# Kernel tuning notes

Hardware: AMD Instinct MI355X
Metric: run time of the kernel (lower is better)

The kernel has to match this reference:

```python
import jax, jax.numpy as jnp
import numpy as np

EPS = 1.1920929e-07  # torch fp32 RMSNorm default eps

def rmsnorm(x, w):
    return x * jax.lax.rsqrt(jnp.mean(x * x, axis=-1, keepdims=True) + EPS) * w

def causal_conv1d(x, w, b):
    # x: [B, L, di], w: [di, dc] depthwise kernel, b: [di]
    di, dc = w.shape
    xt = jnp.swapaxes(x, 1, 2)                       # [B, di, L]
    xt = jnp.pad(xt, ((0, 0), (0, 0), (dc - 1, 0)))  # causal left pad
    out = jax.lax.conv_general_dilated(
        xt, w[:, None, :], window_strides=(1,), padding='VALID',
        feature_group_count=di, dimension_numbers=('NCH', 'OIH', 'NCH'))
    return jnp.swapaxes(out + b[None, :, None], 1, 2)  # [B, L, di]

def selective_scan(u, dt, Bm, Cm, A, Dp):
    # u, dt: [B, L, di]; Bm, Cm: [B, L, ds]; A: [di, ds]; Dp: [di]
    Bsz, L, di = u.shape
    ds = A.shape[1]
    def step(h, inp):
        dt_t, B_t, C_t, u_t = inp
        dA = jnp.exp(dt_t[..., None] * A)                           # [B, di, ds]
        dBu = dt_t[..., None] * B_t[:, None, :] * u_t[..., None]    # [B, di, ds]
        h = dA * h + dBu
        y = jnp.einsum('bds,bs->bd', h, C_t)
        return h, y
    h0 = jnp.zeros((Bsz, di, ds), u.dtype)
    xs = (jnp.swapaxes(dt, 0, 1), jnp.swapaxes(Bm, 0, 1),
          jnp.swapaxes(Cm, 0, 1), jnp.swapaxes(u, 0, 1))
    _, ys = jax.lax.scan(step, h0, xs)                # ys: [L, B, di]
    return jnp.swapaxes(ys, 0, 1) + u * Dp            # skip connection D*u

def mamba_block(x, in_w, cw, cb, xp_w, dtp_w, dtp_b, a_log, dp, out_w, d_state, dt_rank):
    di = a_log.shape[0]
    xz = jnp.einsum('bld,ed->ble', x, in_w)           # [B, L, 2*di]
    x_in, z = xz[..., :di], xz[..., di:]
    xc = jax.nn.silu(causal_conv1d(x_in, cw, cb))     # [B, L, di]
    x_dbl = jnp.einsum('bld,ed->ble', xc, xp_w)       # [B, L, dt_rank+2*ds]
    dt = x_dbl[..., :dt_rank]
    Bm = x_dbl[..., dt_rank:dt_rank + d_state]
    Cm = x_dbl[..., dt_rank + d_state:]
    dt = jax.nn.softplus(jnp.einsum('blr,dr->bld', dt, dtp_w) + dtp_b)
    A = -jnp.exp(a_log)                               # [di, ds]
    y = selective_scan(xc, dt, Bm, Cm, A, dp)
    y = y * jax.nn.silu(z)
    return jnp.einsum('bld,ed->ble', y, out_w)        # [B, L, d_model]

def mlp(x, w1, b1, w2, b2):
    h = jax.nn.gelu(jnp.einsum('bld,ed->ble', x, w1) + b1, approximate=False)
    return jax.nn.gelu(jnp.einsum('ble,de->bld', h, w2) + b2, approximate=False)

def reference(x, in_proj_w, conv_w, conv_b, x_proj_w, dt_proj_w, dt_proj_b,
              A_log, D_param, out_proj_w, mlp_w1, mlp_b1, mlp_w2, mlp_b2,
              ln_w, ln2_w):
    d_state = A_log.shape[-1]
    dt_rank = dt_proj_w.shape[-1]
    num_layers = in_proj_w.shape[0]
    residual2 = x
    for i in range(num_layers):
        residual = x
        x = mamba_block(x, in_proj_w[i], conv_w[i], conv_b[i], x_proj_w[i],
                        dt_proj_w[i], dt_proj_b[i], A_log[i], D_param[i],
                        out_proj_w[i], d_state, dt_rank)
        x = mlp(x, mlp_w1, mlp_b1, mlp_w2, mlp_b2)
        x = rmsnorm(x + residual, ln_w)
    return rmsnorm(x + residual2, ln2_w)

def setup_inputs() -> dict:
    key = jax.random.key(0)
    ks = jax.random.split(key, 16)
    B, L, D = 4, 2048, 1024
    NL, di, ds, dc, dtr = 2, 2048, 16, 4, 64
    s = 0.02
    return {
        'x': jax.random.normal(ks[0], (B, L, D), jnp.float32),
        'in_proj_w': jax.random.normal(ks[1], (NL, 2 * di, D), jnp.float32) * s,
        'conv_w': jax.random.normal(ks[2], (NL, di, dc), jnp.float32) * 0.3,
        'conv_b': jax.random.normal(ks[3], (NL, di), jnp.float32) * 0.02,
        'x_proj_w': jax.random.normal(ks[4], (NL, dtr + 2 * ds, di), jnp.float32) * s,
        'dt_proj_w': jax.random.normal(ks[5], (NL, di, dtr), jnp.float32) * 0.1,
        'dt_proj_b': jax.random.normal(ks[6], (NL, di), jnp.float32) * 0.5 - 4.0,
        'A_log': jnp.log(jax.random.uniform(ks[7], (NL, di, ds), jnp.float32, 1.0, 16.0)),
        'D_param': jax.random.normal(ks[8], (NL, di), jnp.float32),
        'out_proj_w': jax.random.normal(ks[9], (NL, D, di), jnp.float32) * s,
        'mlp_w1': jax.random.normal(ks[10], (2 * D, D), jnp.float32) * s,
        'mlp_b1': jnp.zeros((2 * D,), jnp.float32),
        'mlp_w2': jax.random.normal(ks[11], (D, 2 * D), jnp.float32) * s,
        'mlp_b2': jnp.zeros((D,), jnp.float32),
        'ln_w': jnp.ones((D,), jnp.float32),
        'ln2_w': jnp.ones((D,), jnp.float32),
    }
```

## Files before the change

### kernel.cpp

```cpp
#include <hip/hip_runtime.h>
#include <math.h>

namespace {

constexpr int Bsz = 4;
constexpr int L   = 2048;
constexpr int D   = 1024;
constexpr int DI  = 2048;
constexpr int DSTATE = 16;
constexpr int DTR = 64;
constexpr int ML  = Bsz * L;
constexpr int NCH = 32;
constexpr int CL  = 64;

typedef __attribute__((ext_vector_type(8))) short bfrag;
typedef __attribute__((ext_vector_type(4))) float f32x4;

__device__ __forceinline__ unsigned short f2b(float f) {
  union { float f; unsigned int u; } c; c.f = f;
  unsigned int u = c.u;
  unsigned int r = (u + 0x7fffu + ((u >> 16) & 1u)) >> 16;
  return (unsigned short)r;
}
__device__ __forceinline__ float b2f(unsigned short h) {
  union { unsigned int u; float f; } c; c.u = ((unsigned int)h) << 16;
  return c.f;
}

__device__ __forceinline__ void async16(const void* g, void* l) {
  __builtin_amdgcn_global_load_lds(
      (const __attribute__((address_space(1))) void*)g,
      (__attribute__((address_space(3))) void*)l, 16, 0, 0);
}

template<int ACT>
__device__ __forceinline__ float activate(float x) {
  if (ACT == 1) { return x / (1.f + expf(-x)); }
  if (ACT == 2) { return 0.5f * x * (1.f + erff(x * 0.7071067811865475f)); }
  if (ACT == 3) { return (x > 20.f) ? x : log1pf(expf(x)); }
  return x;
}

template<int ACT, bool HAS_BIAS, int BN, bool SPLIT>
__global__ __launch_bounds__(512) void gemm2(
    const unsigned short* __restrict__ A, long lda,
    const unsigned short* __restrict__ W, long ldw,
    const float* __restrict__ bias,
    unsigned short* __restrict__ C0,
    unsigned short* __restrict__ C1,
    long ldc, int K)
{
  constexpr int NB   = BN / 64;
  constexpr int ABUF = 256 * 64;
  constexpr int BBUF = BN * 64;
  constexpr int NLA  = 4;
  constexpr int NLB  = NB;
  constexpr int NL   = NLA + NLB;
  __shared__ unsigned short lds[2 * ABUF + 2 * BBUF];

  const int tid  = threadIdx.x;
  const int lane = tid & 63;
  const int wid  = tid >> 6;
  const int wr   = wid >> 2;
  const int wc   = wid & 3;
  const int frow = lane & 15;
  const int klg  = lane >> 4;

  const int gx = gridDim.x;
  int id = blockIdx.y * gx + blockIdx.x;
  const int q = (gx * gridDim.y) >> 3;
  id = (id & 7) * q + (id >> 3);
  const int bx = id % gx;
  const int by = id / gx;
  const long bm = (long)by * 256;
  const long bn = (long)bx * BN;

  unsigned short* Cb;
  long cbase;
  if (SPLIT) {
    if (bn < 2048) { Cb = C0; cbase = bn; }
    else           { Cb = C1; cbase = bn - 2048; }
  } else { Cb = C0; cbase = bn; }

  f32x4 acc[8][NB];
  #pragma unroll
  for (int m = 0; m < 8; ++m)
    #pragma unroll
    for (int n = 0; n < NB; ++n)
      acc[m][n] = (f32x4){0.f, 0.f, 0.f, 0.f};

  auto stage = [&](int kt, int p) {
    const long kcol = (long)kt * 64;
    #pragma unroll
    for (int l = 0; l < NLA; ++l) {
      const int idx = tid + l * 512;
      const int row = idx >> 3;
      const int ch  = (idx & 7) ^ (row & 7);
      async16(A + (bm + row) * lda + kcol + ch * 8,
              &lds[p * ABUF + idx * 8]);
    }
    #pragma unroll
    for (int l = 0; l < NLB; ++l) {
      const int idx = tid + l * 512;
      const int row = idx >> 3;
      const int ch  = (idx & 7) ^ (row & 7);
      async16(W + (bn + row) * ldw + kcol + ch * 8,
              &lds[2 * ABUF + p * BBUF + idx * 8]);
    }
  };

  const int NT = K >> 6;
  stage(0, 0);
  stage(1, 1);
  asm volatile("s_waitcnt vmcnt(%0)" :: "n"(NL) : "memory");
  __builtin_amdgcn_sched_barrier(0);
  __builtin_amdgcn_s_barrier();

  for (int kt = 0; kt < NT; ++kt) {
    const unsigned short* Ab = &lds[(kt & 1) * ABUF];
    const unsigned short* Bb = &lds[2 * ABUF + (kt & 1) * BBUF];
    __builtin_amdgcn_s_setprio(1);
    #pragma unroll
    for (int kk = 0; kk < 2; ++kk) {
      bfrag av[8], bv[NB];
      #pragma unroll
      for (int m = 0; m < 8; ++m) {
        const int r  = wr * 128 + m * 16 + frow;
        const int ch = (kk * 4 + klg) ^ (r & 7);
        av[m] = *reinterpret_cast<const bfrag*>(&Ab[r * 64 + ch * 8]);
      }
      #pragma unroll
      for (int n = 0; n < NB; ++n) {
        const int r  = wc * (BN / 4) + n * 16 + frow;
        const int ch = (kk * 4 + klg) ^ (r & 7);
        bv[n] = *reinterpret_cast<const bfrag*>(&Bb[r * 64 + ch * 8]);
      }
      #pragma unroll
      for (int m = 0; m < 8; ++m)
        #pragma unroll
        for (int n = 0; n < NB; ++n)
          acc[m][n] = __builtin_amdgcn_mfma_f32_16x16x32_bf16(bv[n], av[m], acc[m][n], 0, 0, 0);
    }
    __builtin_amdgcn_s_setprio(0);
    if (kt + 1 == NT) break;
    __builtin_amdgcn_sched_barrier(0);
    __builtin_amdgcn_s_barrier();
    if (kt + 2 < NT) {
      stage(kt + 2, kt & 1);
      asm volatile("s_waitcnt vmcnt(%0)" :: "n"(NL) : "memory");
    } else {
      asm volatile("s_waitcnt vmcnt(0)" ::: "memory");
    }
    __builtin_amdgcn_sched_barrier(0);
    __builtin_amdgcn_s_barrier();
  }

  #pragma unroll
  for (int n = 0; n < NB; ++n) {
    const long coff = wc * (BN / 4) + n * 16 + klg * 4;
    float4 b4 = make_float4(0.f, 0.f, 0.f, 0.f);
    if (HAS_BIAS) b4 = *reinterpret_cast<const float4*>(&bias[bn + coff]);
    #pragma unroll
    for (int m = 0; m < 8; ++m) {
      const long row = bm + wr * 128 + m * 16 + frow;
      const float v0 = activate<ACT>(acc[m][n][0] + b4.x);
      const float v1 = activate<ACT>(acc[m][n][1] + b4.y);
      const float v2 = activate<ACT>(acc[m][n][2] + b4.z);
      const float v3 = activate<ACT>(acc[m][n][3] + b4.w);
      ushort4 o; o.x = f2b(v0); o.y = f2b(v1); o.z = f2b(v2); o.w = f2b(v3);
      *reinterpret_cast<ushort4*>(&Cb[row * ldc + cbase + coff]) = o;
    }
  }
}

template<int ACT, bool HAS_BIAS>
__global__ __launch_bounds__(256) void gemm_mfma(
    const unsigned short* __restrict__ A, long lda,
    const unsigned short* __restrict__ W, long ldw,
    const float* __restrict__ bias,
    unsigned short* __restrict__ C, long ldc,
    int K)
{
  __shared__ unsigned short As[128 * 32];
  __shared__ unsigned short Bs[128 * 32];
  const int tid  = threadIdx.x;
  const int lane = tid & 63;
  const int w    = tid >> 6;
  const int wr   = w >> 1, wc = w & 1;
  const long bm = (long)blockIdx.y * 128;
  const long bn = (long)blockIdx.x * 128;

  const int srow = tid >> 2;
  const int scol = (tid & 3) * 8;
  const unsigned short* ga0 = A + (bm + srow)      * lda + scol;
  const unsigned short* ga1 = A + (bm + 64 + srow) * lda + scol;
  const unsigned short* gb0 = W + (bn + srow)      * ldw + scol;
  const unsigned short* gb1 = W + (bn + 64 + srow) * ldw + scol;
  char* lA = (char*)As;
  char* lB = (char*)Bs;
  const int loff = tid * 16;

  const int frow = lane & 15;
  const int klg  = lane >> 4;
  const int fko  = klg * 8;

  f32x4 acc[4][4];
  #pragma unroll
  for (int m = 0; m < 4; ++m)
    #pragma unroll
    for (int n = 0; n < 4; ++n)
      acc[m][n] = (f32x4){0.f, 0.f, 0.f, 0.f};

  for (int k0 = 0; k0 < K; k0 += 32) {
    __syncthreads();
    async16(ga0 + k0, lA + loff);
    async16(ga1 + k0, lA + 4096 + loff);
    async16(gb0 + k0, lB + loff);
    async16(gb1 + k0, lB + 4096 + loff);
    __syncthreads();
    bfrag a[4], b[4];
    #pragma unroll
    for (int m = 0; m < 4; ++m)
      a[m] = *reinterpret_cast<const bfrag*>(&As[(wr*64 + m*16 + frow)*32 + fko]);
    #pragma unroll
    for (int n = 0; n < 4; ++n)
      b[n] = *reinterpret_cast<const bfrag*>(&Bs[(wc*64 + n*16 + frow)*32 + fko]);
    #pragma unroll
    for (int m = 0; m < 4; ++m)
      #pragma unroll
      for (int n = 0; n < 4; ++n)
        acc[m][n] = __builtin_amdgcn_mfma_f32_16x16x32_bf16(b[n], a[m], acc[m][n], 0, 0, 0);
  }

  #pragma unroll
  for (int n = 0; n < 4; ++n) {
    const long col = bn + wc*64 + n*16 + klg*4;
    float4 b4 = make_float4(0.f, 0.f, 0.f, 0.f);
    if (HAS_BIAS) b4 = *reinterpret_cast<const float4*>(&bias[col]);
    #pragma unroll
    for (int m = 0; m < 4; ++m) {
      const long row = bm + wr*64 + m*16 + frow;
      const float v0 = activate<ACT>(acc[m][n][0] + b4.x);
      const float v1 = activate<ACT>(acc[m][n][1] + b4.y);
      const float v2 = activate<ACT>(acc[m][n][2] + b4.z);
      const float v3 = activate<ACT>(acc[m][n][3] + b4.w);
      ushort4 o; o.x = f2b(v0); o.y = f2b(v1); o.z = f2b(v2); o.w = f2b(v3);
      *reinterpret_cast<ushort4*>(&C[row * ldc + col]) = o;
    }
  }
}

__global__ __launch_bounds__(256) void xproj_mfma(
    const unsigned short* __restrict__ A,
    const unsigned short* __restrict__ W,
    float* __restrict__ xdbl,
    unsigned short* __restrict__ dtr)
{
  __shared__ unsigned short As[64 * 32];
  __shared__ unsigned short Bs[96 * 32];
  const int tid  = threadIdx.x;
  const int lane = tid & 63;
  const int wv   = tid >> 6;
  const long bm  = (long)blockIdx.x * 64;

  const int acol = (tid & 3) * 8;
  const unsigned short* ga  = A + (bm + (tid >> 2)) * DI + acol;
  const unsigned short* gb0 = W + (long)(tid >> 2) * DI + acol;
  const unsigned short* gb1 = W + (long)((tid >> 2) + 64) * DI + acol;
  char* lA = (char*)As;
  char* lB = (char*)Bs;

  const int frow = lane & 15;
  const int klg  = lane >> 4;
  const int fko  = klg * 8;

  f32x4 acc[6];
  #pragma unroll
  for (int n = 0; n < 6; ++n) acc[n] = (f32x4){0.f, 0.f, 0.f, 0.f};

  for (int k0 = 0; k0 < DI; k0 += 32) {
    __syncthreads();
    async16(ga + k0, lA + tid * 16);
    async16(gb0 + k0, lB + tid * 16);
    if (tid < 128) async16(gb1 + k0, lB + 4096 + tid * 16);
    __syncthreads();
    const bfrag a = *reinterpret_cast<const bfrag*>(&As[(wv*16 + frow)*32 + fko]);
    #pragma unroll
    for (int n = 0; n < 6; ++n) {
      const bfrag b = *reinterpret_cast<const bfrag*>(&Bs[(n*16 + frow)*32 + fko]);
      acc[n] = __builtin_amdgcn_mfma_f32_16x16x32_bf16(b, a, acc[n], 0, 0, 0);
    }
  }

  const long row = bm + wv*16 + frow;
  #pragma unroll
  for (int n = 0; n < 6; ++n) {
    const int col = n*16 + klg*4;
    float4 v; v.x = acc[n][0]; v.y = acc[n][1]; v.z = acc[n][2]; v.w = acc[n][3];
    *reinterpret_cast<float4*>(&xdbl[row * 96 + col]) = v;
    if (n < 4) {
      ushort4 o; o.x = f2b(v.x); o.y = f2b(v.y); o.z = f2b(v.z); o.w = f2b(v.w);
      *reinterpret_cast<ushort4*>(&dtr[row * 64 + col]) = o;
    }
  }
}

__global__ __launch_bounds__(256) void cvt_bf16(
    const float* __restrict__ in, unsigned short* __restrict__ out, long n4)
{
  const long i = (long)blockIdx.x * 256 + threadIdx.x;
  if (i < n4) {
    const float4 v = reinterpret_cast<const float4*>(in)[i];
    ushort4 o; o.x = f2b(v.x); o.y = f2b(v.y); o.z = f2b(v.z); o.w = f2b(v.w);
    reinterpret_cast<ushort4*>(out)[i] = o;
  }
}

__global__ __launch_bounds__(256) void conv_silu(
    const unsigned short* __restrict__ xin,
    const float* __restrict__ w,
    const float* __restrict__ bias,
    unsigned short* __restrict__ xc)
{
  const int idx = blockIdx.x * 256 + threadIdx.x;
  const int D4 = DI / 4;
  const int d  = (idx % D4) * 4;
  const int bt = idx / D4;
  const int t  = bt & (L - 1);
  const int b  = bt >> 11;
  const float4 w0 = *reinterpret_cast<const float4*>(w + (long)(d+0)*4);
  const float4 w1 = *reinterpret_cast<const float4*>(w + (long)(d+1)*4);
  const float4 w2 = *reinterpret_cast<const float4*>(w + (long)(d+2)*4);
  const float4 w3 = *reinterpret_cast<const float4*>(w + (long)(d+3)*4);
  const float4 bv = *reinterpret_cast<const float4*>(bias + d);
  float a0 = bv.x, a1 = bv.y, a2 = bv.z, a3 = bv.w;
  const float wk0[4] = {w0.x, w0.y, w0.z, w0.w};
  const float wk1[4] = {w1.x, w1.y, w1.z, w1.w};
  const float wk2[4] = {w2.x, w2.y, w2.z, w2.w};
  const float wk3[4] = {w3.x, w3.y, w3.z, w3.w};
  #pragma unroll
  for (int k = 0; k < 4; ++k) {
    const int tt = t - 3 + k;
    if (tt >= 0) {
      const ushort4 xv = *reinterpret_cast<const ushort4*>(xin + ((long)(b * L + tt)) * DI + d);
      a0 = fmaf(wk0[k], b2f(xv.x), a0);
      a1 = fmaf(wk1[k], b2f(xv.y), a1);
      a2 = fmaf(wk2[k], b2f(xv.z), a2);
      a3 = fmaf(wk3[k], b2f(xv.w), a3);
    }
  }
  a0 = a0 / (1.f + expf(-a0));
  a1 = a1 / (1.f + expf(-a1));
  a2 = a2 / (1.f + expf(-a2));
  a3 = a3 / (1.f + expf(-a3));
  ushort4 o; o.x = f2b(a0); o.y = f2b(a1); o.z = f2b(a2); o.w = f2b(a3);
  *reinterpret_cast<ushort4*>(xc + (long)bt * DI + d) = o;
}

__global__ __launch_bounds__(256) void scan_p1(
    const unsigned short* __restrict__ dt,
    const unsigned short* __restrict__ u,
    const float* __restrict__ xdbl,
    const float* __restrict__ a_log,
    float* __restrict__ hend,
    float* __restrict__ sdt)
{
  const int bid = blockIdx.x;
  const int dg = bid & 7;
  const int c  = (bid >> 3) & (NCH - 1);
  const int b  = bid >> 8;
  const int d  = dg * 256 + threadIdx.x;
  float A[16];
  #pragma unroll
  for (int q = 0; q < 4; ++q) {
    const float4 al = *reinterpret_cast<const float4*>(a_log + (long)d * 16 + q * 4);
    A[q*4+0] = -__expf(al.x); A[q*4+1] = -__expf(al.y);
    A[q*4+2] = -__expf(al.z); A[q*4+3] = -__expf(al.w);
  }
  float h[16];
  #pragma unroll
  for (int s = 0; s < 16; ++s) h[s] = 0.f;
  float s_dt = 0.f;
  const long row0 = (long)b * L + (long)c * CL;
  for (int t = 0; t < CL; ++t) {
    const long row = row0 + t;
    const float dtv = b2f(dt[row * DI + d]);
    const float uv  = b2f(u [row * DI + d]);
    const float* bp = xdbl + row * 96 + 64;
    const float4 B0 = *reinterpret_cast<const float4*>(bp + 0);
    const float4 B1 = *reinterpret_cast<const float4*>(bp + 4);
    const float4 B2 = *reinterpret_cast<const float4*>(bp + 8);
    const float4 B3 = *reinterpret_cast<const float4*>(bp + 12);
    const float Bv[16] = {B0.x,B0.y,B0.z,B0.w, B1.x,B1.y,B1.z,B1.w,
                          B2.x,B2.y,B2.z,B2.w, B3.x,B3.y,B3.z,B3.w};
    s_dt += dtv;
    const float dtu = dtv * uv;
    #pragma unroll
    for (int s = 0; s < 16; ++s)
      h[s] = fmaf(__expf(dtv * A[s]), h[s], dtu * Bv[s]);
  }
  const long cb = (long)(b * NCH + c);
  #pragma unroll
  for (int s = 0; s < 16; ++s)
    hend[(cb * 16 + s) * DI + d] = h[s];
  sdt[cb * DI + d] = s_dt;
}

__global__ __launch_bounds__(256) void scan_p2(
    float* __restrict__ hend,
    const float* __restrict__ sdt,
    const float* __restrict__ a_log)
{
  const long idx = (long)blockIdx.x * 256 + threadIdx.x;
  const int d = idx & (DI - 1);
  const int s = (idx >> 11) & 15;
  const int b = idx >> 15;
  const float A = -__expf(a_log[(long)d * 16 + s]);
  float h = 0.f;
  for (int c = 0; c < NCH; ++c) {
    const long cb = (long)(b * NCH + c);
    const long off = (cb * 16 + s) * DI + d;
    const float hl = hend[off];
    const float sd = sdt[cb * DI + d];
    hend[off] = h;
    h = fmaf(__expf(A * sd), h, hl);
  }
}

__global__ __launch_bounds__(256) void scan_p3(
    const unsigned short* __restrict__ dt,
    const unsigned short* __restrict__ u,
    const float* __restrict__ xdbl,
    const unsigned short* __restrict__ z,
    const float* __restrict__ a_log,
    const float* __restrict__ dpar,
    const float* __restrict__ hinit,
    unsigned short* __restrict__ y)
{
  const int bid = blockIdx.x;
  const int dg = bid & 7;
  const int c  = (bid >> 3) & (NCH - 1);
  const int b  = bid >> 8;
  const int d  = dg * 256 + threadIdx.x;
  float A[16];
  #pragma unroll
  for (int q = 0; q < 4; ++q) {
    const float4 al = *reinterpret_cast<const float4*>(a_log + (long)d * 16 + q * 4);
    A[q*4+0] = -__expf(al.x); A[q*4+1] = -__expf(al.y);
    A[q*4+2] = -__expf(al.z); A[q*4+3] = -__expf(al.w);
  }
  const float Dv = dpar[d];
  const long cb = (long)(b * NCH + c);
  float h[16];
  #pragma unroll
  for (int s = 0; s < 16; ++s)
    h[s] = hinit[(cb * 16 + s) * DI + d];
  const long row0 = (long)b * L + (long)c * CL;
  for (int t = 0; t < CL; ++t) {
    const long row = row0 + t;
    const float dtv = b2f(dt[row * DI + d]);
    const float uv  = b2f(u [row * DI + d]);
    const float* bp = xdbl + row * 96 + 64;
    const float4 B0 = *reinterpret_cast<const float4*>(bp + 0);
    const float4 B1 = *reinterpret_cast<const float4*>(bp + 4);
    const float4 B2 = *reinterpret_cast<const float4*>(bp + 8);
    const float4 B3 = *reinterpret_cast<const float4*>(bp + 12);
    const float4 C0 = *reinterpret_cast<const float4*>(bp + 16);
    const float4 C1 = *reinterpret_cast<const float4*>(bp + 20);
    const float4 C2 = *reinterpret_cast<const float4*>(bp + 24);
    const float4 C3 = *reinterpret_cast<const float4*>(bp + 28);
    const float Bv[16] = {B0.x,B0.y,B0.z,B0.w, B1.x,B1.y,B1.z,B1.w,
                          B2.x,B2.y,B2.z,B2.w, B3.x,B3.y,B3.z,B3.w};
    const float Cv[16] = {C0.x,C0.y,C0.z,C0.w, C1.x,C1.y,C1.z,C1.w,
                          C2.x,C2.y,C2.z,C2.w, C3.x,C3.y,C3.z,C3.w};
    const float dtu = dtv * uv;
    float yv = 0.f;
    #pragma unroll
    for (int s = 0; s < 16; ++s) {
      h[s] = fmaf(__expf(dtv * A[s]), h[s], dtu * Bv[s]);
      yv = fmaf(h[s], Cv[s], yv);
    }
    const float zv = b2f(z[row * DI + d]);
    const float sg = zv / (1.f + __expf(-zv));
    y[row * DI + d] = f2b(fmaf(uv, Dv, yv) * sg);
  }
}

template<bool BIN, bool WBF>
__global__ __launch_bounds__(256) void add_rmsnorm(
    const void* __restrict__ xinp, const float* __restrict__ res,
    const float* __restrict__ w, float* __restrict__ out,
    unsigned short* __restrict__ xb)
{
  const int row = blockIdx.x;
  const int tid = threadIdx.x;
  const long base = (long)row * D;
  float4 v;
  if (BIN) {
    const ushort4 t = *reinterpret_cast<const ushort4*>((const unsigned short*)xinp + base + tid * 4);
    v.x = b2f(t.x); v.y = b2f(t.y); v.z = b2f(t.z); v.w = b2f(t.w);
  } else {
    v = *reinterpret_cast<const float4*>((const float*)xinp + base + tid * 4);
  }
  const float4 r = *reinterpret_cast<const float4*>(res + base + tid * 4);
  v.x += r.x; v.y += r.y; v.z += r.z; v.w += r.w;
  float ss = v.x*v.x + v.y*v.y + v.z*v.z + v.w*v.w;
  #pragma unroll
  for (int m = 1; m < 64; m <<= 1) ss += __shfl_xor(ss, m);
  __shared__ float red[4];
  if ((tid & 63) == 0) red[tid >> 6] = ss;
  __syncthreads();
  const float tot = red[0] + red[1] + red[2] + red[3];
  const float scale = rsqrtf(tot * (1.f / (float)D) + 1.1920929e-07f);
  const float4 wv = *reinterpret_cast<const float4*>(w + tid * 4);
  float4 o;
  o.x = v.x * scale * wv.x;
  o.y = v.y * scale * wv.y;
  o.z = v.z * scale * wv.z;
  o.w = v.w * scale * wv.w;
  *reinterpret_cast<float4*>(out + base + tid * 4) = o;
  if (WBF) {
    ushort4 ob; ob.x = f2b(o.x); ob.y = f2b(o.y); ob.z = f2b(o.z); ob.w = f2b(o.w);
    *reinterpret_cast<ushort4*>(xb + base + tid * 4) = ob;
  }
}

}

extern "C" void kernel_launch(void* const* d_in, const int* in_sizes, int n_in,
                              void* d_out, int out_size, void* d_ws, size_t ws_size,
                              hipStream_t stream)
{
  const float* x0     = (const float*)d_in[0];
  const float* in_w   = (const float*)d_in[1];
  const float* conv_w = (const float*)d_in[2];
  const float* conv_b = (const float*)d_in[3];
  const float* xp_w   = (const float*)d_in[4];
  const float* dtp_w  = (const float*)d_in[5];
  const float* dtp_b  = (const float*)d_in[6];
  const float* a_log  = (const float*)d_in[7];
  const float* d_par  = (const float*)d_in[8];
  const float* out_w  = (const float*)d_in[9];
  const float* w1     = (const float*)d_in[10];
  const float* b1     = (const float*)d_in[11];
  const float* w2     = (const float*)d_in[12];
  const float* b2     = (const float*)d_in[13];
  const float* ln_w   = (const float*)d_in[14];
  const float* ln2_w  = (const float*)d_in[15];
  float* out = (float*)d_out;

  char* ws = (char*)d_ws;
  unsigned short* in_wb  = (unsigned short*)(ws);
  unsigned short* out_wb = (unsigned short*)(ws + (16UL  << 20));
  unsigned short* w1b    = (unsigned short*)(ws + (24UL  << 20));
  unsigned short* w2b    = (unsigned short*)(ws + (28UL  << 20));
  unsigned short* xbf    = (unsigned short*)(ws + (32UL  << 20));
  unsigned short* zb     = (unsigned short*)(ws + (48UL  << 20));
  unsigned short* xc     = (unsigned short*)(ws + (80UL  << 20));
  float*          xdbl   = (float*)(ws + (112UL << 20));
  float*          sdtb   = (float*)(ws + (115UL << 20));
  float*          hendb  = (float*)(ws + (116UL << 20));
  unsigned short* xinb   = (unsigned short*)(ws + (132UL << 20));
  unsigned short* dtb    = xinb;
  unsigned short* ybf    = (unsigned short*)(ws + (164UL << 20));
  unsigned short* hm     = ybf;
  unsigned short* mo     = (unsigned short*)(ws + (196UL << 20));
  unsigned short* t2     = mo;
  unsigned short* xp_wb  = (unsigned short*)(ws + (212UL << 20));
  unsigned short* dtp_wb = (unsigned short*)(ws + (213UL << 20));
  unsigned short* dtrb   = (unsigned short*)(ws + (214UL << 20));

  const dim3 blk(256);
  const dim3 blk5(512);

  cvt_bf16<<<dim3((2L*2*DI*D/4 + 255)/256), blk, 0, stream>>>(in_w,  in_wb,  2L*2*DI*D/4);
  cvt_bf16<<<dim3((2L*D*DI/4   + 255)/256), blk, 0, stream>>>(out_w, out_wb, 2L*D*DI/4);
  cvt_bf16<<<dim3((2L*D*D/4    + 255)/256), blk, 0, stream>>>(w1,    w1b,    2L*D*D/4);
  cvt_bf16<<<dim3((2L*D*D/4    + 255)/256), blk, 0, stream>>>(w2,    w2b,    2L*D*D/4);
  cvt_bf16<<<dim3((2L*96*DI/4  + 255)/256), blk, 0, stream>>>(xp_w,  xp_wb,  2L*96*DI/4);
  cvt_bf16<<<dim3((2L*DI*DTR/4 + 255)/256), blk, 0, stream>>>(dtp_w, dtp_wb, 2L*DI*DTR/4);
  cvt_bf16<<<dim3(((long)ML*D/4+ 255)/256), blk, 0, stream>>>(x0,    xbf,    (long)ML*D/4);

  const float* xcur = x0;
  for (int layer = 0; layer < 2; ++layer) {
    const long lo = (long)layer;
    const unsigned short* Winb = in_wb + lo * 2 * DI * D;
    gemm2<0,false,256,true><<<dim3(16, 32), blk5, 0, stream>>>(
        xbf, D, Winb, D, nullptr, xinb, zb, DI, D);
    conv_silu<<<dim3((long)ML*DI/4/256), blk, 0, stream>>>(
        xinb, conv_w + lo*DI*4, conv_b + lo*DI, xc);
    xproj_mfma<<<dim3(ML/64), blk, 0, stream>>>(
        xc, xp_wb + lo*96*DI, xdbl, dtrb);
    gemm_mfma<3,true><<<dim3(DI/128, ML/128), blk, 0, stream>>>(
        dtrb, DTR, dtp_wb + lo*DI*DTR, DTR, dtp_b + lo*DI, dtb, DI, DTR);
    scan_p1<<<dim3(Bsz*NCH*(DI/256)), blk, 0, stream>>>(
        dtb, xc, xdbl, a_log + lo*DI*DSTATE, hendb, sdtb);
    scan_p2<<<dim3(Bsz*DSTATE*DI/256), blk, 0, stream>>>(
        hendb, sdtb, a_log + lo*DI*DSTATE);
    scan_p3<<<dim3(Bsz*NCH*(DI/256)), blk, 0, stream>>>(
        dtb, xc, xdbl, zb, a_log + lo*DI*DSTATE, d_par + lo*DI, hendb, ybf);
    gemm2<0,false,128,false><<<dim3(8, 32), blk5, 0, stream>>>(
        ybf, DI, out_wb + lo*D*DI, DI, nullptr, mo, nullptr, D, DI);
    gemm2<2,true,256,false><<<dim3(8, 32), blk5, 0, stream>>>(
        mo, D, w1b, D, b1, hm, nullptr, 2*D, D);
    gemm2<2,true,128,false><<<dim3(8, 32), blk5, 0, stream>>>(
        hm, 2*D, w2b, 2*D, b2, t2, nullptr, D, 2*D);
    add_rmsnorm<true,true><<<dim3(ML), blk, 0, stream>>>(t2, xcur, ln_w, out, xbf);
    xcur = out;
  }
  add_rmsnorm<false,false><<<dim3(ML), blk, 0, stream>>>(out, x0, ln2_w, out, nullptr);
}
```

Before: 1.114 ms.

## Shrink GEMM tiles to 128x128, pipeline xproj, merge bf16 conversions

Reworks the main GEMM kernel from 256xBN tiles with 512 threads to fixed 128x128 tiles with 256 threads, giving more blocks per GEMM and so more CUs in use, at the cost of less data reuse per block. It also moves the x-projection kernel to a double-buffered, swizzled 64-wide-K async pipeline in place of its fully synchronised 32-wide loop. Finally, it merges the seven weight and input bf16 conversion launches into a single kernel to cut launch overhead.

```diff
diff --git a/kernel.cpp b/kernel.cpp
--- a/kernel.cpp
+++ b/kernel.cpp
@@ -41,8 +41,8 @@
   return x;
 }
 
-template<int ACT, bool HAS_BIAS, int BN, bool SPLIT>
-__global__ __launch_bounds__(512) void gemm2(
+template<int ACT, bool HAS_BIAS, bool SPLIT>
+__global__ __launch_bounds__(256) void gemm2(
     const unsigned short* __restrict__ A, long lda,
     const unsigned short* __restrict__ W, long ldw,
     const float* __restrict__ bias,
@@ -50,19 +50,16 @@
     unsigned short* __restrict__ C1,
     long ldc, int K)
 {
-  constexpr int NB   = BN / 64;
-  constexpr int ABUF = 256 * 64;
-  constexpr int BBUF = BN * 64;
-  constexpr int NLA  = 4;
-  constexpr int NLB  = NB;
-  constexpr int NL   = NLA + NLB;
+  constexpr int ABUF = 128 * 64;
+  constexpr int BBUF = 128 * 64;
+  constexpr int NL   = 8;
   __shared__ unsigned short lds[2 * ABUF + 2 * BBUF];
 
   const int tid  = threadIdx.x;
   const int lane = tid & 63;
   const int wid  = tid >> 6;
-  const int wr   = wid >> 2;
-  const int wc   = wid & 3;
+  const int wr   = wid >> 1;
+  const int wc   = wid & 1;
   const int frow = lane & 15;
   const int klg  = lane >> 4;
 
@@ -72,8 +69,8 @@
   id = (id & 7) * q + (id >> 3);
   const int bx = id % gx;
   const int by = id / gx;
-  const long bm = (long)by * 256;
-  const long bn = (long)bx * BN;
+  const long bm = (long)by * 128;
+  const long bn = (long)bx * 128;
 
   unsigned short* Cb;
   long cbase;
@@ -82,26 +79,26 @@
     else           { Cb = C1; cbase = bn - 2048; }
   } else { Cb = C0; cbase = bn; }
 
-  f32x4 acc[8][NB];
-  #pragma unroll
-  for (int m = 0; m < 8; ++m)
-    #pragma unroll
-    for (int n = 0; n < NB; ++n)
+  f32x4 acc[4][4];
+  #pragma unroll
+  for (int m = 0; m < 4; ++m)
+    #pragma unroll
+    for (int n = 0; n < 4; ++n)
       acc[m][n] = (f32x4){0.f, 0.f, 0.f, 0.f};
 
   auto stage = [&](int kt, int p) {
     const long kcol = (long)kt * 64;
     #pragma unroll
-    for (int l = 0; l < NLA; ++l) {
-      const int idx = tid + l * 512;
+    for (int l = 0; l < 4; ++l) {
+      const int idx = tid + l * 256;
       const int row = idx >> 3;
       const int ch  = (idx & 7) ^ (row & 7);
       async16(A + (bm + row) * lda + kcol + ch * 8,
               &lds[p * ABUF + idx * 8]);
     }
     #pragma unroll
-    for (int l = 0; l < NLB; ++l) {
-      const int idx = tid + l * 512;
+    for (int l = 0; l < 4; ++l) {
+      const int idx = tid + l * 256;
       const int row = idx >> 3;
       const int ch  = (idx & 7) ^ (row & 7);
       async16(W + (bn + row) * ldw + kcol + ch * 8,
@@ -122,23 +119,23 @@
     __builtin_amdgcn_s_setprio(1);
     #pragma unroll
     for (int kk = 0; kk < 2; ++kk) {
-      bfrag av[8], bv[NB];
+      bfrag av[4], bv[4];
       #pragma unroll
-      for (int m = 0; m < 8; ++m) {
-        const int r  = wr * 128 + m * 16 + frow;
+      for (int m = 0; m < 4; ++m) {
+        const int r  = wr * 64 + m * 16 + frow;
         const int ch = (kk * 4 + klg) ^ (r & 7);
         av[m] = *reinterpret_cast<const bfrag*>(&Ab[r * 64 + ch * 8]);
       }
       #pragma unroll
-      for (int n = 0; n < NB; ++n) {
-        const int r  = wc * (BN / 4) + n * 16 + frow;
+      for (int n = 0; n < 4; ++n) {
+        const int r  = wc * 64 + n * 16 + frow;
         const int ch = (kk * 4 + klg) ^ (r & 7);
         bv[n] = *reinterpret_cast<const bfrag*>(&Bb[r * 64 + ch * 8]);
       }
       #pragma unroll
-      for (int m = 0; m < 8; ++m)
+      for (int m = 0; m < 4; ++m)
         #pragma unroll
-        for (int n = 0; n < NB; ++n)
+        for (int n = 0; n < 4; ++n)
           acc[m][n] = __builtin_amdgcn_mfma_f32_16x16x32_bf16(bv[n], av[m], acc[m][n], 0, 0, 0);
     }
     __builtin_amdgcn_s_setprio(0);
@@ -156,13 +153,13 @@
   }
 
   #pragma unroll
-  for (int n = 0; n < NB; ++n) {
-    const long coff = wc * (BN / 4) + n * 16 + klg * 4;
+  for (int n = 0; n < 4; ++n) {
+    const long coff = wc * 64 + n * 16 + klg * 4;
     float4 b4 = make_float4(0.f, 0.f, 0.f, 0.f);
     if (HAS_BIAS) b4 = *reinterpret_cast<const float4*>(&bias[bn + coff]);
     #pragma unroll
-    for (int m = 0; m < 8; ++m) {
-      const long row = bm + wr * 128 + m * 16 + frow;
+    for (int m = 0; m < 4; ++m) {
+      const long row = bm + wr * 64 + m * 16 + frow;
       const float v0 = activate<ACT>(acc[m][n][0] + b4.x);
       const float v1 = activate<ACT>(acc[m][n][1] + b4.y);
       const float v2 = activate<ACT>(acc[m][n][2] + b4.z);
@@ -256,40 +253,78 @@
     float* __restrict__ xdbl,
     unsigned short* __restrict__ dtr)
 {
-  __shared__ unsigned short As[64 * 32];
-  __shared__ unsigned short Bs[96 * 32];
+  constexpr int ABUF = 64 * 64;
+  constexpr int BBUF = 96 * 64;
+  constexpr int NL   = 5;
+  __shared__ unsigned short lds[2 * ABUF + 2 * BBUF];
+
   const int tid  = threadIdx.x;
   const int lane = tid & 63;
   const int wv   = tid >> 6;
-  const long bm  = (long)blockIdx.x * 64;
-
-  const int acol = (tid & 3) * 8;
-  const unsigned short* ga  = A + (bm + (tid >> 2)) * DI + acol;
-  const unsigned short* gb0 = W + (long)(tid >> 2) * DI + acol;
-  const unsigned short* gb1 = W + (long)((tid >> 2) + 64) * DI + acol;
-  char* lA = (char*)As;
-  char* lB = (char*)Bs;
-
   const int frow = lane & 15;
   const int klg  = lane >> 4;
-  const int fko  = klg * 8;
+  const long bm  = (long)blockIdx.x * 64;
 
   f32x4 acc[6];
   #pragma unroll
   for (int n = 0; n < 6; ++n) acc[n] = (f32x4){0.f, 0.f, 0.f, 0.f};
 
-  for (int k0 = 0; k0 < DI; k0 += 32) {
-    __syncthreads();
-    async16(ga + k0, lA + tid * 16);
-    async16(gb0 + k0, lB + tid * 16);
-    if (tid < 128) async16(gb1 + k0, lB + 4096 + tid * 16);
-    __syncthreads();
-    const bfrag a = *reinterpret_cast<const bfrag*>(&As[(wv*16 + frow)*32 + fko]);
-    #pragma unroll
-    for (int n = 0; n < 6; ++n) {
-      const bfrag b = *reinterpret_cast<const bfrag*>(&Bs[(n*16 + frow)*32 + fko]);
-      acc[n] = __builtin_amdgcn_mfma_f32_16x16x32_bf16(b, a, acc[n], 0, 0, 0);
-    }
+  auto stage = [&](int kt, int p) {
+    const long kcol = (long)kt * 64;
+    #pragma unroll
+    for (int l = 0; l < 2; ++l) {
+      const int idx = tid + l * 256;
+      const int row = idx >> 3;
+      const int ch  = (idx & 7) ^ (row & 7);
+      async16(A + (bm + row) * DI + kcol + ch * 8,
+              &lds[p * ABUF + idx * 8]);
+    }
+    #pragma unroll
+    for (int l = 0; l < 3; ++l) {
+      const int idx = tid + l * 256;
+      const int row = idx >> 3;
+      const int ch  = (idx & 7) ^ (row & 7);
+      async16(W + (long)row * DI + kcol + ch * 8,
+              &lds[2 * ABUF + p * BBUF + idx * 8]);
+    }
+  };
+
+  constexpr int NT = DI / 64;
+  stage(0, 0);
+  stage(1, 1);
+  asm volatile("s_waitcnt vmcnt(%0)" :: "n"(NL) : "memory");
+  __builtin_amdgcn_sched_barrier(0);
+  __builtin_amdgcn_s_barrier();
+
+  for (int kt = 0; kt < NT; ++kt) {
+    const unsigned short* Ab = &lds[(kt & 1) * ABUF];
+    const unsigned short* Bb = &lds[2 * ABUF + (kt & 1) * BBUF];
+    __builtin_amdgcn_s_setprio(1);
+    #pragma unroll
+    for (int kk = 0; kk < 2; ++kk) {
+      const int ra = wv * 16 + frow;
+      const int cha = (kk * 4 + klg) ^ (ra & 7);
+      const bfrag a = *reinterpret_cast<const bfrag*>(&Ab[ra * 64 + cha * 8]);
+      #pragma unroll
+      for (int n = 0; n < 6; ++n) {
+        const int rb = n * 16 + frow;
+        const int chb = (kk * 4 + klg) ^ (rb & 7);
+        const bfrag b = *reinterpret_cast<const bfrag*>(&Bb[rb * 64 + chb * 8]);
+        acc[n] = __builtin_amdgcn_mfma_f32_16x16x32_bf16(b, a, acc[n], 0, 0, 0);
+      }
+    }
+    __builtin_amdgcn_s_setprio(0);
+    if (kt + 1 == NT) break;
+    __builtin_amdgcn_sched_barrier(0);
+    __builtin_amdgcn_s_barrier();
+    if (kt + 2 < NT) {
+      stage(kt + 2, kt & 1);
+      asm volatile("s_waitcnt vmcnt(%0)" :: "n"(NL) : "memory");
+    } else {
+      asm volatile("s_waitcnt vmcnt(0)" ::: "memory");
+    }
+    __builtin_amdgcn_sched_barrier(0);
+    __builtin_amdgcn_s_barrier();
   }
 
   const long row = bm + wv*16 + frow;
@@ -305,15 +340,28 @@
   }
 }
 
-__global__ __launch_bounds__(256) void cvt_bf16(
-    const float* __restrict__ in, unsigned short* __restrict__ out, long n4)
-{
-  const long i = (long)blockIdx.x * 256 + threadIdx.x;
-  if (i < n4) {
-    const float4 v = reinterpret_cast<const float4*>(in)[i];
-    ushort4 o; o.x = f2b(v.x); o.y = f2b(v.y); o.z = f2b(v.z); o.w = f2b(v.w);
-    reinterpret_cast<ushort4*>(out)[i] = o;
-  }
+__global__ __launch_bounds__(256) void cvt_all(
+    const float* __restrict__ s0, unsigned short* __restrict__ d0, long n0,
+    const float* __restrict__ s1, unsigned short* __restrict__ d1, long n1,
+    const float* __restrict__ s2, unsigned short* __restrict__ d2, long n2,
+    const float* __restrict__ s3, unsigned short* __restrict__ d3, long n3,
+    const float* __restrict__ s4, unsigned short* __restrict__ d4, long n4,
+    const float* __restrict__ s5, unsigned short* __restrict__ d5, long n5,
+    const float* __restrict__ s6, unsigned short* __restrict__ d6, long n6)
+{
+  long i = (long)blockIdx.x * 256 + threadIdx.x;
+  const float* s; unsigned short* d;
+  if      (i < n0)                    { s = s0; d = d0; }
+  else if ((i -= n0) < n1)            { s = s1; d = d1; }
+  else if ((i -= n1) < n2)            { s = s2; d = d2; }
+  else if ((i -= n2) < n3)            { s = s3; d = d3; }
+  else if ((i -= n3) < n4)            { s = s4; d = d4; }
+  else if ((i -= n4) < n5)            { s = s5; d = d5; }
+  else if ((i -= n5) < n6)            { s = s6; d = d6; }
+  else return;
+  const float4 v = reinterpret_cast<const float4*>(s)[i];
+  ushort4 o; o.x = f2b(v.x); o.y = f2b(v.y); o.z = f2b(v.z); o.w = f2b(v.w);
+  reinterpret_cast<ushort4*>(d)[i] = o;
 }
 
 __global__ __launch_bounds__(256) void conv_silu(
@@ -571,21 +619,21 @@
   unsigned short* dtrb   = (unsigned short*)(ws + (214UL << 20));
 
   const dim3 blk(256);
-  const dim3 blk5(512);
-
-  cvt_bf16<<<dim3((2L*2*DI*D/4 + 255)/256), blk, 0, stream>>>(in_w,  in_wb,  2L*2*DI*D/4);
-  cvt_bf16<<<dim3((2L*D*DI/4   + 255)/256), blk, 0, stream>>>(out_w, out_wb, 2L*D*DI/4);
-  cvt_bf16<<<dim3((2L*D*D/4    + 255)/256), blk, 0, stream>>>(w1,    w1b,    2L*D*D/4);
-  cvt_bf16<<<dim3((2L*D*D/4    + 255)/256), blk, 0, stream>>>(w2,    w2b,    2L*D*D/4);
-  cvt_bf16<<<dim3((2L*96*DI/4  + 255)/256), blk, 0, stream>>>(xp_w,  xp_wb,  2L*96*DI/4);
-  cvt_bf16<<<dim3((2L*DI*DTR/4 + 255)/256), blk, 0, stream>>>(dtp_w, dtp_wb, 2L*DI*DTR/4);
-  cvt_bf16<<<dim3(((long)ML*D/4+ 255)/256), blk, 0, stream>>>(x0,    xbf,    (long)ML*D/4);
+
+  {
+    const long n0 = 2L*2*DI*D/4, n1 = 2L*D*DI/4, n2 = 2L*D*D/4, n3 = 2L*D*D/4;
+    const long n4 = 2L*96*DI/4,  n5 = 2L*DI*DTR/4, n6 = (long)ML*D/4;
+    const long tot = n0+n1+n2+n3+n4+n5+n6;
+    cvt_all<<<dim3((tot + 255)/256), blk, 0, stream>>>(
+        in_w, in_wb, n0,  out_w, out_wb, n1,  w1, w1b, n2,  w2, w2b, n3,
+        xp_w, xp_wb, n4,  dtp_w, dtp_wb, n5,  x0, xbf, n6);
+  }
 
   const float* xcur = x0;
   for (int layer = 0; layer < 2; ++layer) {
     const long lo = (long)layer;
     const unsigned short* Winb = in_wb + lo * 2 * DI * D;
-    gemm2<0,false,256,true><<<dim3(16, 32), blk5, 0, stream>>>(
+    gemm2<0,false,true><<<dim3(32, 64), blk, 0, stream>>>(
         xbf, D, Winb, D, nullptr, xinb, zb, DI, D);
     conv_silu<<<dim3((long)ML*DI/4/256), blk, 0, stream>>>(
         xinb, conv_w + lo*DI*4, conv_b + lo*DI, xc);
@@ -599,11 +647,11 @@
         hendb, sdtb, a_log + lo*DI*DSTATE);
     scan_p3<<<dim3(Bsz*NCH*(DI/256)), blk, 0, stream>>>(
         dtb, xc, xdbl, zb, a_log + lo*DI*DSTATE, d_par + lo*DI, hendb, ybf);
-    gemm2<0,false,128,false><<<dim3(8, 32), blk5, 0, stream>>>(
+    gemm2<0,false,false><<<dim3(8, 64), blk, 0, stream>>>(
         ybf, DI, out_wb + lo*D*DI, DI, nullptr, mo, nullptr, D, DI);
-    gemm2<2,true,256,false><<<dim3(8, 32), blk5, 0, stream>>>(
+    gemm2<2,true,false><<<dim3(16, 64), blk, 0, stream>>>(
         mo, D, w1b, D, b1, hm, nullptr, 2*D, D);
-    gemm2<2,true,128,false><<<dim3(8, 32), blk5, 0, stream>>>(
+    gemm2<2,true,false><<<dim3(8, 64), blk, 0, stream>>>(
         hm, 2*D, w2b, 2*D, b2, t2, nullptr, D, 2*D);
     add_rmsnorm<true,true><<<dim3(ML), blk, 0, stream>>>(t2, xcur, ln_w, out, xbf);
     xcur = out;
```

Measured after the change: 1.132 ms. Within noise of the previous version (+1.6%).
